# Kernel tuning notes

Measured on AMD Instinct MI355X. Metric: run time of the kernel, lower is better.

Reference implementation:

```python
import jax, jax.numpy as jnp
import numpy as np

B, S, D = 4, 2048, 1024
H, DK, DV = 16, 64, 64
NEG = -10000.0
EPS = 1e-5


def setup_inputs() -> dict:
    key = jax.random.key(0)
    ks = jax.random.split(key, 12)
    inp = {
        "q": jax.random.normal(ks[0], (B, S, D), jnp.float32),
        "k": jax.random.normal(ks[1], (B, S, D), jnp.float32),
        "v": jax.random.normal(ks[2], (B, S, D), jnp.float32),
        "mask": jax.random.randint(ks[3], (B, S, S), 0, 2, jnp.int32),
        # linear layers: y = x @ W.T + b (torch convention)
        "Wq": jax.random.normal(ks[4], (H * DK, D), jnp.float32) * (D ** -0.5),
        "bq": jnp.zeros((H * DK,), jnp.float32),
        "Wk": jax.random.normal(ks[5], (H * DK, D), jnp.float32) * (D ** -0.5),
        "bk": jnp.zeros((H * DK,), jnp.float32),
        "Wv": jax.random.normal(ks[6], (H * DV, D), jnp.float32) * (D ** -0.5),
        "bv": jnp.zeros((H * DV,), jnp.float32),
        "ln_g": jnp.ones((D,), jnp.float32),
        "ln_b": jnp.zeros((D,), jnp.float32),
    }
    return inp


def reference(q, k, v, mask, Wq, bq, Wk, bk, Wv, bv, ln_g, ln_b):
    residual = q
    # project and split heads -> [B, H, S, dk]
    qh = (q @ Wq.T + bq).reshape(B, S, H, DK).transpose(0, 2, 1, 3)
    kh = (k @ Wk.T + bk).reshape(B, S, H, DK).transpose(0, 2, 1, 3)
    vh = (v @ Wv.T + bv).reshape(B, S, H, DV).transpose(0, 2, 1, 3)

    scale = DK ** -0.5
    attn = jnp.einsum("bhqd,bhkd->bhqk", qh * scale, kh)  # [B,H,S,S]
    # padding mask adder: (1 - mask) * -1e4, broadcast over heads
    attn = attn + (1.0 - mask.astype(attn.dtype))[:, None, :, :] * NEG
    # causal mask adder
    causal = jnp.tril(jnp.ones((S, S), attn.dtype))
    attn = attn + (1.0 - causal) * NEG
    attn = jax.nn.softmax(attn, axis=-1)

    out = jnp.einsum("bhqk,bhkd->bhqd", attn, vh)  # [B,H,S,dv]
    out = out.transpose(0, 2, 1, 3).reshape(B, S, H * DV)
    out = out + residual
    # layer norm (eps=1e-5)
    mu = jnp.mean(out, axis=-1, keepdims=True)
    var = jnp.mean(jnp.square(out - mu), axis=-1, keepdims=True)
    out = (out - mu) * jax.lax.rsqrt(var + EPS) * ln_g + ln_b
    return out, attn
```

## Files before the change

kernel.cpp:

```cpp
#include <hip/hip_runtime.h>

typedef __bf16 bf16;
typedef float f32x4 __attribute__((ext_vector_type(4)));
typedef bf16 bf16x8 __attribute__((ext_vector_type(8)));
typedef bf16 bf16x4 __attribute__((ext_vector_type(4)));

constexpr int Bc = 4, Sc = 2048, Dc = 1024, Hc = 16, DKc = 64;
constexpr float NEGc = -10000.0f;

__global__ __launch_bounds__(256, 2) void proj_kernel(
    const float* __restrict__ xq, const float* __restrict__ xk, const float* __restrict__ xv,
    const float* __restrict__ Wq, const float* __restrict__ bq,
    const float* __restrict__ Wk, const float* __restrict__ bk,
    const float* __restrict__ Wv, const float* __restrict__ bv,
    bf16* __restrict__ qh, bf16* __restrict__ kh, bf16* __restrict__ vh)
{
    const int z = blockIdx.z;
    const float* x    = (z == 0) ? xq : (z == 1) ? xk : xv;
    const float* W    = (z == 0) ? Wq : (z == 1) ? Wk : Wv;
    const float* bias = (z == 0) ? bq : (z == 1) ? bk : bv;
    bf16* dst         = (z == 0) ? qh : (z == 1) ? kh : vh;

    const int tid = threadIdx.x;
    const int wave = tid >> 6, lane = tid & 63, quad = lane >> 4, m16 = lane & 15;
    const int wm = (wave >> 1) * 64, wn = (wave & 1) * 64;
    const int m0 = blockIdx.y * 128, n0 = blockIdx.x * 128;

    __shared__ bf16 As[128][40];
    __shared__ bf16 Bs[128][40];

    const f32x4 zero4 = {0.f, 0.f, 0.f, 0.f};
    f32x4 acc[4][4];
#pragma unroll
    for (int i = 0; i < 4; i++)
#pragma unroll
        for (int j = 0; j < 4; j++) acc[i][j] = zero4;

    for (int kk = 0; kk < 32; ++kk) {
        const int k0 = kk * 32;
#pragma unroll
        for (int i = 0; i < 4; i++) {
            int f4 = tid + i * 256;
            int r = f4 >> 3, c4 = (f4 & 7) * 4;
            float4 a = *(const float4*)&x[(size_t)(m0 + r) * Dc + k0 + c4];
            float4 w = *(const float4*)&W[(size_t)(n0 + r) * Dc + k0 + c4];
            bf16x4 av; av.x = (bf16)a.x; av.y = (bf16)a.y; av.z = (bf16)a.z; av.w = (bf16)a.w;
            bf16x4 wv; wv.x = (bf16)w.x; wv.y = (bf16)w.y; wv.z = (bf16)w.z; wv.w = (bf16)w.w;
            *(bf16x4*)&As[r][c4] = av;
            *(bf16x4*)&Bs[r][c4] = wv;
        }
        __syncthreads();
        bf16x8 af[4], bfr[4];
#pragma unroll
        for (int t = 0; t < 4; t++) {
            af[t]  = *(const bf16x8*)&As[wm + t * 16 + m16][quad * 8];
            bfr[t] = *(const bf16x8*)&Bs[wn + t * 16 + m16][quad * 8];
        }
#pragma unroll
        for (int mt = 0; mt < 4; mt++)
#pragma unroll
            for (int nt = 0; nt < 4; nt++)
                acc[mt][nt] = __builtin_amdgcn_mfma_f32_16x16x32_bf16(af[mt], bfr[nt], acc[mt][nt], 0, 0, 0);
        __syncthreads();
    }

#pragma unroll
    for (int nt = 0; nt < 4; nt++) {
        int n = n0 + wn + nt * 16 + m16;
        float bval = bias[n];
        int h = n >> 6, d = n & 63;
#pragma unroll
        for (int mt = 0; mt < 4; mt++) {
#pragma unroll
            for (int r = 0; r < 4; r++) {
                int m = m0 + wm + mt * 16 + quad * 4 + r;
                int bb = m >> 11, s = m & 2047;
                float val = acc[mt][nt][r] + bval;
                dst[(((size_t)(bb * Hc + h)) * Sc + s) * DKc + d] = (bf16)val;
            }
        }
    }
}

__global__ __launch_bounds__(256) void vtrans_kernel(const bf16* __restrict__ vh,
                                                     bf16* __restrict__ vt)
{
    const int tid = threadIdx.x;
    const int bh = blockIdx.y, s0 = blockIdx.x * 64;
    __shared__ bf16 tile[64][72];
    const bf16* src = vh + ((size_t)bh * Sc + s0) * DKc;
#pragma unroll
    for (int i = 0; i < 2; i++) {
        int v = tid + i * 256;
        int sl = v >> 3, d8 = (v & 7) * 8;
        *(bf16x8*)&tile[sl][d8] = *(const bf16x8*)&src[sl * DKc + d8];
    }
    __syncthreads();
#pragma unroll
    for (int i = 0; i < 2; i++) {
        int v = tid + i * 256;
        int d = v >> 3, s8 = (v & 7) * 8;
        bf16x8 o;
#pragma unroll
        for (int j = 0; j < 8; j++) o[j] = tile[s8 + j][d];
        *(bf16x8*)&vt[((size_t)bh * DKc + d) * Sc + s0 + s8] = o;
    }
}

__global__ __launch_bounds__(256, 2) void attn_kernel(
    const bf16* __restrict__ qh, const bf16* __restrict__ kh, const bf16* __restrict__ vt,
    const int* __restrict__ mask, float* __restrict__ attn_out, float* __restrict__ out)
{
    const int qt = blockIdx.x, h = blockIdx.y, b = blockIdx.z;
    const int bh = b * Hc + h, q0 = qt * 16;
    const int tid = threadIdx.x;
    const int wave = tid >> 6, lane = tid & 63, quad = lane >> 4, m16 = lane & 15;

    __shared__ bf16 sc[16][2048];
    float* red = reinterpret_cast<float*>(&sc[0][0]);

    const bf16* qrow = qh + ((size_t)bh * Sc + q0) * DKc;
    const bf16* krow = kh + (size_t)bh * Sc * DKc;
    const bf16* vrow = vt + (size_t)bh * DKc * Sc;

    const bf16x8 aq0 = *(const bf16x8*)&qrow[m16 * DKc + quad * 8];
    const bf16x8 aq1 = *(const bf16x8*)&qrow[m16 * DKc + 32 + quad * 8];

    const f32x4 zero4 = {0.f, 0.f, 0.f, 0.f};
    f32x4 acc[32];
#pragma unroll
    for (int t = 0; t < 32; t++) acc[t] = zero4;

#pragma unroll
    for (int t = 0; t < 32; t++) {
        const int n0 = (t * 4 + wave) * 16;
        const bf16* kb = &krow[(size_t)(n0 + m16) * DKc + quad * 8];
        bf16x8 b0 = *(const bf16x8*)kb;
        bf16x8 b1 = *(const bf16x8*)(kb + 32);
        acc[t] = __builtin_amdgcn_mfma_f32_16x16x32_bf16(aq0, b0, acc[t], 0, 0, 0);
        acc[t] = __builtin_amdgcn_mfma_f32_16x16x32_bf16(aq1, b1, acc[t], 0, 0, 0);
    }

    float rmax[4] = {-3e38f, -3e38f, -3e38f, -3e38f};
#pragma unroll
    for (int t = 0; t < 32; t++) {
        const int kcol = (t * 4 + wave) * 16 + m16;
#pragma unroll
        for (int r = 0; r < 4; r++) {
            const int grow = q0 + quad * 4 + r;
            const int mv = mask[((size_t)b * Sc + grow) * Sc + kcol];
            float s = acc[t][r] * 0.125f;
            s += (mv == 0) ? NEGc : 0.f;
            s += (kcol > grow) ? NEGc : 0.f;
            acc[t][r] = s;
            rmax[r] = fmaxf(rmax[r], s);
        }
    }
#pragma unroll
    for (int off = 1; off < 16; off <<= 1)
#pragma unroll
        for (int r = 0; r < 4; r++) rmax[r] = fmaxf(rmax[r], __shfl_xor(rmax[r], off, 64));
    if (m16 == 0) {
#pragma unroll
        for (int r = 0; r < 4; r++) red[wave * 16 + quad * 4 + r] = rmax[r];
    }
    __syncthreads();
#pragma unroll
    for (int r = 0; r < 4; r++) {
        const int row = quad * 4 + r;
        rmax[r] = fmaxf(fmaxf(red[row], red[16 + row]), fmaxf(red[32 + row], red[48 + row]));
    }

    float rsum[4] = {0.f, 0.f, 0.f, 0.f};
#pragma unroll
    for (int t = 0; t < 32; t++)
#pragma unroll
        for (int r = 0; r < 4; r++) {
            float e = __expf(acc[t][r] - rmax[r]);
            acc[t][r] = e;
            rsum[r] += e;
        }
#pragma unroll
    for (int off = 1; off < 16; off <<= 1)
#pragma unroll
        for (int r = 0; r < 4; r++) rsum[r] += __shfl_xor(rsum[r], off, 64);
    if (m16 == 0) {
#pragma unroll
        for (int r = 0; r < 4; r++) red[64 + wave * 16 + quad * 4 + r] = rsum[r];
    }
    __syncthreads();
    float inv[4];
#pragma unroll
    for (int r = 0; r < 4; r++) {
        const int row = quad * 4 + r;
        inv[r] = 1.0f / (red[64 + row] + red[80 + row] + red[96 + row] + red[112 + row]);
    }
    __syncthreads();

    float* arow_base = attn_out + ((size_t)bh * Sc + q0) * Sc;
#pragma unroll
    for (int t = 0; t < 32; t++) {
        const int kcol = (t * 4 + wave) * 16 + m16;
#pragma unroll
        for (int r = 0; r < 4; r++) {
            const int row = quad * 4 + r;
            const float p = acc[t][r] * inv[r];
            arow_base[(size_t)row * Sc + kcol] = p;
            sc[row][kcol ^ ((row & 7) << 3)] = (bf16)p;
        }
    }
    __syncthreads();

    const int dcol = wave * 16 + m16;
    const bf16* vbase = &vrow[(size_t)dcol * Sc];
    f32x4 oacc = zero4;
#pragma unroll 8
    for (int ks = 0; ks < 64; ks++) {
        const int k0 = ks * 32 + quad * 8;
        bf16x8 a  = *(const bf16x8*)&sc[m16][k0 ^ ((m16 & 7) << 3)];
        bf16x8 bv8 = *(const bf16x8*)&vbase[k0];
        oacc = __builtin_amdgcn_mfma_f32_16x16x32_bf16(a, bv8, oacc, 0, 0, 0);
    }
    float* obase = out + ((size_t)(b * Sc + q0)) * Dc + h * DKc;
#pragma unroll
    for (int r = 0; r < 4; r++) {
        const int row = quad * 4 + r;
        obase[(size_t)row * Dc + dcol] = oacc[r];
    }
}

__global__ __launch_bounds__(256) void ln_kernel(float* __restrict__ out,
                                                 const float* __restrict__ resid,
                                                 const float* __restrict__ gw,
                                                 const float* __restrict__ bw)
{
    const int row = blockIdx.x, tid = threadIdx.x;
    float* orow = out + (size_t)row * Dc;
    const float* rrow = resid + (size_t)row * Dc;
    float4 x = *(const float4*)&orow[tid * 4];
    float4 rr = *(const float4*)&rrow[tid * 4];
    x.x += rr.x; x.y += rr.y; x.z += rr.z; x.w += rr.w;
    float s1 = x.x + x.y + x.z + x.w;
    float s2 = x.x * x.x + x.y * x.y + x.z * x.z + x.w * x.w;
#pragma unroll
    for (int off = 1; off < 64; off <<= 1) {
        s1 += __shfl_xor(s1, off, 64);
        s2 += __shfl_xor(s2, off, 64);
    }
    __shared__ float red[8];
    const int wave = tid >> 6, lane = tid & 63;
    if (lane == 0) { red[wave] = s1; red[4 + wave] = s2; }
    __syncthreads();
    s1 = red[0] + red[1] + red[2] + red[3];
    s2 = red[4] + red[5] + red[6] + red[7];
    const float mu = s1 * (1.f / Dc);
    const float var = s2 * (1.f / Dc) - mu * mu;
    const float rstd = rsqrtf(var + 1e-5f);
    float4 g4 = *(const float4*)&gw[tid * 4];
    float4 b4 = *(const float4*)&bw[tid * 4];
    float4 y;
    y.x = (x.x - mu) * rstd * g4.x + b4.x;
    y.y = (x.y - mu) * rstd * g4.y + b4.y;
    y.z = (x.z - mu) * rstd * g4.z + b4.z;
    y.w = (x.w - mu) * rstd * g4.w + b4.w;
    *(float4*)&orow[tid * 4] = y;
}

extern "C" void kernel_launch(void* const* d_in, const int* in_sizes, int n_in,
                              void* d_out, int out_size, void* d_ws, size_t ws_size,
                              hipStream_t stream)
{
    (void)in_sizes; (void)n_in; (void)out_size; (void)ws_size;
    const float* q    = (const float*)d_in[0];
    const float* k    = (const float*)d_in[1];
    const float* v    = (const float*)d_in[2];
    const int*   mask = (const int*)d_in[3];
    const float* Wq   = (const float*)d_in[4];
    const float* bq   = (const float*)d_in[5];
    const float* Wk   = (const float*)d_in[6];
    const float* bk   = (const float*)d_in[7];
    const float* Wv   = (const float*)d_in[8];
    const float* bv   = (const float*)d_in[9];
    const float* g    = (const float*)d_in[10];
    const float* bet  = (const float*)d_in[11];

    float* out  = (float*)d_out;
    float* attn = out + (size_t)Bc * Sc * Dc;

    const size_t headN = (size_t)Bc * Hc * Sc * DKc;
    bf16* qh = (bf16*)d_ws;
    bf16* kh = qh + headN;
    bf16* vh = kh + headN;
    bf16* vt = vh + headN;

    proj_kernel<<<dim3(8, 64, 3), 256, 0, stream>>>(q, k, v, Wq, bq, Wk, bk, Wv, bv, qh, kh, vh);
    vtrans_kernel<<<dim3(Sc / 64, Bc * Hc), 256, 0, stream>>>(vh, vt);
    attn_kernel<<<dim3(Sc / 16, Hc, Bc), 256, 0, stream>>>(qh, kh, vt, mask, attn, out);
    ln_kernel<<<dim3(Bc * Sc), 256, 0, stream>>>(out, q, g, bet);
}
```

Before: 1.818 ms.

## Skip causally masked key tiles in attention with fallback for fully-masked rows

Attention now computes QK^T, softmax and PV only for key tiles at or below the diagonal, and writes zeros to the upper-triangle attn output with nontemporal stores. If any row's max is very negative (all visible keys padded), it falls back to computing the full row so the softmax stays exact. Shared memory shrinks to a 16x256 chunked buffer so three blocks can share a CU, and q-tiles are launched in reverse so the heavy ones start first. The cost is extra control flow and syncs per chunk, and the zero-fill relies on exp underflowing for causally masked entries.

Result: faster. 1.751 ms (-3.7%).

```diff
diff --git a/kernel.cpp b/kernel.cpp
--- a/kernel.cpp
+++ b/kernel.cpp
@@ -107,21 +107,23 @@
     }
 }
 
-__global__ __launch_bounds__(256, 2) void attn_kernel(
+__global__ __launch_bounds__(256, 3) void attn_kernel(
     const bf16* __restrict__ qh, const bf16* __restrict__ kh, const bf16* __restrict__ vt,
     const int* __restrict__ mask, float* __restrict__ attn_out, float* __restrict__ out)
 {
-    const int qt = blockIdx.x, h = blockIdx.y, b = blockIdx.z;
-    const int bh = b * Hc + h, q0 = qt * 16;
+    const int qtr = (int)gridDim.x - 1 - (int)blockIdx.x;
+    const int h = blockIdx.y, b = blockIdx.z;
+    const int bh = b * Hc + h, q0 = qtr * 16;
     const int tid = threadIdx.x;
     const int wave = tid >> 6, lane = tid & 63, quad = lane >> 4, m16 = lane & 15;
 
-    __shared__ bf16 sc[16][2048];
-    float* red = reinterpret_cast<float*>(&sc[0][0]);
+    __shared__ bf16 sc[16][256];
+    __shared__ float red[128];
 
     const bf16* qrow = qh + ((size_t)bh * Sc + q0) * DKc;
     const bf16* krow = kh + (size_t)bh * Sc * DKc;
     const bf16* vrow = vt + (size_t)bh * DKc * Sc;
+    const int*  mrow = mask + (size_t)b * Sc * Sc;
 
     const bf16x8 aq0 = *(const bf16x8*)&qrow[m16 * DKc + quad * 8];
     const bf16x8 aq1 = *(const bf16x8*)&qrow[m16 * DKc + 32 + quad * 8];
@@ -131,29 +133,40 @@
 #pragma unroll
     for (int t = 0; t < 32; t++) acc[t] = zero4;
 
+    const int gq = qtr >> 4;
+
+#pragma unroll
+    for (int g = 0; g < 8; g++) {
+        if (g <= gq) {
+#pragma unroll
+            for (int tp = 0; tp < 4; tp++) {
+                const int t = g * 4 + tp;
+                const int n0 = (t * 4 + wave) * 16;
+                const bf16* kb = &krow[(size_t)(n0 + m16) * DKc + quad * 8];
+                bf16x8 b0 = *(const bf16x8*)kb;
+                bf16x8 b1 = *(const bf16x8*)(kb + 32);
+                acc[t] = __builtin_amdgcn_mfma_f32_16x16x32_bf16(aq0, b0, acc[t], 0, 0, 0);
+                acc[t] = __builtin_amdgcn_mfma_f32_16x16x32_bf16(aq1, b1, acc[t], 0, 0, 0);
+            }
+        }
+    }
+
+    float rmax[4] = {-3e38f, -3e38f, -3e38f, -3e38f};
 #pragma unroll
     for (int t = 0; t < 32; t++) {
-        const int n0 = (t * 4 + wave) * 16;
-        const bf16* kb = &krow[(size_t)(n0 + m16) * DKc + quad * 8];
-        bf16x8 b0 = *(const bf16x8*)kb;
-        bf16x8 b1 = *(const bf16x8*)(kb + 32);
-        acc[t] = __builtin_amdgcn_mfma_f32_16x16x32_bf16(aq0, b0, acc[t], 0, 0, 0);
-        acc[t] = __builtin_amdgcn_mfma_f32_16x16x32_bf16(aq1, b1, acc[t], 0, 0, 0);
-    }
-
-    float rmax[4] = {-3e38f, -3e38f, -3e38f, -3e38f};
-#pragma unroll
-    for (int t = 0; t < 32; t++) {
-        const int kcol = (t * 4 + wave) * 16 + m16;
-#pragma unroll
-        for (int r = 0; r < 4; r++) {
-            const int grow = q0 + quad * 4 + r;
-            const int mv = mask[((size_t)b * Sc + grow) * Sc + kcol];
-            float s = acc[t][r] * 0.125f;
-            s += (mv == 0) ? NEGc : 0.f;
-            s += (kcol > grow) ? NEGc : 0.f;
-            acc[t][r] = s;
-            rmax[r] = fmaxf(rmax[r], s);
+        const int j = t * 4 + wave;
+        if (j <= qtr) {
+            const int kcol = j * 16 + m16;
+#pragma unroll
+            for (int r = 0; r < 4; r++) {
+                const int grow = q0 + quad * 4 + r;
+                const int mv = mrow[(size_t)grow * Sc + kcol];
+                float s = acc[t][r] * 0.125f;
+                s += (mv == 0) ? NEGc : 0.f;
+                s += (kcol > grow) ? NEGc : 0.f;
+                acc[t][r] = s;
+                rmax[r] = fmaxf(rmax[r], s);
+            }
         }
     }
 #pragma unroll
@@ -171,15 +184,76 @@
         rmax[r] = fmaxf(fmaxf(red[row], red[16 + row]), fmaxf(red[32 + row], red[48 + row]));
     }
 
+    float mn = fminf(fminf(rmax[0], rmax[1]), fminf(rmax[2], rmax[3]));
+    mn = fminf(mn, __shfl_xor(mn, 16, 64));
+    mn = fminf(mn, __shfl_xor(mn, 32, 64));
+    const bool needfull = (mn <= -5000.0f);
+    int Jmax = qtr;
+
+    if (needfull) {
+        __syncthreads();
+#pragma unroll
+        for (int g = 0; g < 8; g++) {
+            if (g > gq) {
+#pragma unroll
+                for (int tp = 0; tp < 4; tp++) {
+                    const int t = g * 4 + tp;
+                    const int n0 = (t * 4 + wave) * 16;
+                    const bf16* kb = &krow[(size_t)(n0 + m16) * DKc + quad * 8];
+                    bf16x8 b0 = *(const bf16x8*)kb;
+                    bf16x8 b1 = *(const bf16x8*)(kb + 32);
+                    acc[t] = __builtin_amdgcn_mfma_f32_16x16x32_bf16(aq0, b0, acc[t], 0, 0, 0);
+                    acc[t] = __builtin_amdgcn_mfma_f32_16x16x32_bf16(aq1, b1, acc[t], 0, 0, 0);
+                }
+            }
+        }
+#pragma unroll
+        for (int t = 0; t < 32; t++) {
+            const int j = t * 4 + wave;
+            if (j > qtr) {
+                const int kcol = j * 16 + m16;
+#pragma unroll
+                for (int r = 0; r < 4; r++) {
+                    const int grow = q0 + quad * 4 + r;
+                    const int mv = mrow[(size_t)grow * Sc + kcol];
+                    float s = acc[t][r] * 0.125f;
+                    s += (mv == 0) ? NEGc : 0.f;
+                    s += (kcol > grow) ? NEGc : 0.f;
+                    acc[t][r] = s;
+                    rmax[r] = fmaxf(rmax[r], s);
+                }
+            }
+        }
+#pragma unroll
+        for (int off = 1; off < 16; off <<= 1)
+#pragma unroll
+            for (int r = 0; r < 4; r++) rmax[r] = fmaxf(rmax[r], __shfl_xor(rmax[r], off, 64));
+        if (m16 == 0) {
+#pragma unroll
+            for (int r = 0; r < 4; r++) red[wave * 16 + quad * 4 + r] = rmax[r];
+        }
+        __syncthreads();
+#pragma unroll
+        for (int r = 0; r < 4; r++) {
+            const int row = quad * 4 + r;
+            rmax[r] = fmaxf(fmaxf(red[row], red[16 + row]), fmaxf(red[32 + row], red[48 + row]));
+        }
+        Jmax = 127;
+    }
+
     float rsum[4] = {0.f, 0.f, 0.f, 0.f};
 #pragma unroll
-    for (int t = 0; t < 32; t++)
-#pragma unroll
-        for (int r = 0; r < 4; r++) {
-            float e = __expf(acc[t][r] - rmax[r]);
-            acc[t][r] = e;
-            rsum[r] += e;
-        }
+    for (int t = 0; t < 32; t++) {
+        const int j = t * 4 + wave;
+        if (j <= Jmax) {
+#pragma unroll
+            for (int r = 0; r < 4; r++) {
+                float e = __expf(acc[t][r] - rmax[r]);
+                acc[t][r] = e;
+                rsum[r] += e;
+            }
+        }
+    }
 #pragma unroll
     for (int off = 1; off < 16; off <<= 1)
 #pragma unroll
@@ -195,31 +269,71 @@
         const int row = quad * 4 + r;
         inv[r] = 1.0f / (red[64 + row] + red[80 + row] + red[96 + row] + red[112 + row]);
     }
-    __syncthreads();
 
     float* arow_base = attn_out + ((size_t)bh * Sc + q0) * Sc;
 #pragma unroll
     for (int t = 0; t < 32; t++) {
-        const int kcol = (t * 4 + wave) * 16 + m16;
-#pragma unroll
-        for (int r = 0; r < 4; r++) {
-            const int row = quad * 4 + r;
-            const float p = acc[t][r] * inv[r];
-            arow_base[(size_t)row * Sc + kcol] = p;
-            sc[row][kcol ^ ((row & 7) << 3)] = (bf16)p;
-        }
-    }
-    __syncthreads();
+        const int j = t * 4 + wave;
+        if (j <= Jmax) {
+            const int kcol = j * 16 + m16;
+#pragma unroll
+            for (int r = 0; r < 4; r++) {
+                const int row = quad * 4 + r;
+                const float p = acc[t][r] * inv[r];
+                acc[t][r] = p;
+                __builtin_nontemporal_store(p, &arow_base[(size_t)row * Sc + kcol]);
+            }
+        }
+    }
+    if (!needfull) {
+        const int z0 = (qtr + 1) * 16;
+        const int c4n = (Sc - z0) >> 2;
+#pragma unroll
+        for (int r = 0; r < 16; r++) {
+            float* rp = arow_base + (size_t)r * Sc + z0;
+            for (int c = tid; c < c4n; c += 256)
+                __builtin_nontemporal_store(zero4, (f32x4*)(rp + 4 * c));
+        }
+    }
 
     const int dcol = wave * 16 + m16;
     const bf16* vbase = &vrow[(size_t)dcol * Sc];
+    const int swz = (m16 & 7) << 3;
     f32x4 oacc = zero4;
-#pragma unroll 8
-    for (int ks = 0; ks < 64; ks++) {
-        const int k0 = ks * 32 + quad * 8;
-        bf16x8 a  = *(const bf16x8*)&sc[m16][k0 ^ ((m16 & 7) << 3)];
-        bf16x8 bv8 = *(const bf16x8*)&vbase[k0];
-        oacc = __builtin_amdgcn_mfma_f32_16x16x32_bf16(a, bv8, oacc, 0, 0, 0);
+#pragma unroll
+    for (int c = 0; c < 8; c++) {
+        if (c * 16 <= Jmax) {
+            __syncthreads();
+#pragma unroll
+            for (int tp = 0; tp < 4; tp++) {
+                const int t = c * 4 + tp;
+                const int j = t * 4 + wave;
+                const int lc = (tp * 4 + wave) * 16 + m16;
+                if (j <= Jmax) {
+#pragma unroll
+                    for (int r = 0; r < 4; r++) {
+                        const int row = quad * 4 + r;
+                        sc[row][lc ^ ((row & 7) << 3)] = (bf16)acc[t][r];
+                    }
+                } else if (j <= (Jmax | 1)) {
+#pragma unroll
+                    for (int r = 0; r < 4; r++) {
+                        const int row = quad * 4 + r;
+                        sc[row][lc ^ ((row & 7) << 3)] = (bf16)0.f;
+                    }
+                }
+            }
+            __syncthreads();
+#pragma unroll
+            for (int lks = 0; lks < 8; lks++) {
+                if (c * 16 + 2 * lks <= Jmax) {
+                    const int k0 = lks * 32 + quad * 8;
+                    bf16x8 a  = *(const bf16x8*)&sc[m16][k0 ^ swz];
+                    bf16x8 b8 = *(const bf16x8*)&vbase[c * 256 + k0];
+                    oacc = __builtin_amdgcn_mfma_f32_16x16x32_bf16(a, b8, oacc, 0, 0, 0);
+                }
+            }
+        }
     }
     float* obase = out + ((size_t)(b * Sc + q0)) * Dc + h * DKc;
 #pragma unroll
```
